# Optimization experiments

Measured on AMD Instinct MI355X. Metric: run time of the kernel, lower is better.

## Reference

```python
import jax, jax.numpy as jnp
import numpy as np

N_NODES = 8192
N_EDGES = 65536
NB = 10            # number_of_basis
MID = 32           # middle_layer_size
MAX_R = 10.0       # max_radius
NZ, NM = 48, 16    # z / mol embedding sizes -> 64x0e node input
IN_S = NZ + NM     # 64 scalars
H_S, H_V = 32, 8   # hidden irreps 32x0e + 8x1o (dim 56)
O_S = 16           # output irreps 16x0e
W0N = IN_S * H_S + IN_S * H_V                                  # 2560
W1N = H_S*H_S + H_V*H_S + H_S*H_V + H_V*H_V + H_V*H_V          # 1664
W2N = H_S*O_S + H_V*O_S                                        # 640
H_DIM = H_S + 3 * H_V                                          # 56


def _fcnet(e, W1, W2):
    # e3nn FullyConnectedNet([NB, MID, numel], silu): fan-in normalized linears
    h = jax.nn.silu(e @ W1 / np.sqrt(W1.shape[0]))
    return h @ W2 / np.sqrt(W2.shape[0])


def _ln(x, g, b):
    m = jnp.mean(x, -1, keepdims=True)
    v = jnp.var(x, -1, keepdims=True)
    return (x - m) * jax.lax.rsqrt(v + 1e-5) * g + b


def _sus(t):
    # smooth compact-support bump helper: exp(-1/t) for t>0 else 0
    return jnp.where(t > 0, jnp.exp(-1.0 / jnp.where(t > 0, t, 1.0)), 0.0)


def _forward(pos, Ez, Em,
             b0_W1, b0_W2, b0_g, b0_b,
             b1_W1, b1_W2, b1_g, b1_b,
             b2_W1, b2_W2, b2_g, b2_b,
             z, mol_id, edge_src, edge_dst):
    N = pos.shape[0]
    E = edge_src.shape[0]
    avg = E / N  # avg_num_neighbors (static)

    # node embedding: 64x0e
    x = jnp.concatenate([Ez[z], Em[mol_id]], axis=-1)          # [N, 64]

    vec = pos[edge_dst] - pos[edge_src]                        # [E, 3]
    length = jnp.linalg.norm(vec, axis=1)                      # [E]

    # soft_one_hot_linspace(basis='smooth_finite', cutoff=True) * sqrt(NB)
    vals = jnp.linspace(0.0, MAX_R, NB + 2)[1:-1]
    step = MAX_R / (NB + 1)
    u = (length[:, None] - vals) / step
    emb = (1.14136 * np.exp(2.0)) * _sus(u + 1.0) * _sus(1.0 - u)
    emb = emb * np.sqrt(NB)                                    # [E, NB]

    # spherical harmonics lmax=1, normalize=True, 'component' norm
    nrm = vec / jnp.maximum(length, 1e-9)[:, None]
    sh_v = np.sqrt(3.0) * nrm                                  # [E, 3]  (l=1; l=0 comp == 1)

    # ---- interaction block 0: 64x0e -> 32x0e + 8x1o ----
    w = _fcnet(emb, b0_W1, b0_W2)                              # [E, 2560]
    w00 = w[:, :IN_S * H_S].reshape(E, IN_S, H_S)
    w01 = w[:, IN_S * H_S:].reshape(E, IN_S, H_V)
    xe = x[edge_src]                                           # [E, 64]
    es = jnp.einsum('eu,euw->ew', xe, w00) / np.sqrt(IN_S)
    ev = jnp.einsum('eu,euw,ei->ewi', xe, w01, sh_v) / np.sqrt(IN_S)
    msg = jnp.concatenate([es, ev.reshape(E, 3 * H_V)], -1)    # [E, 56]
    x = _ln(jax.ops.segment_sum(msg, edge_dst, num_segments=N) / np.sqrt(avg), b0_g, b0_b)

    # ---- interaction block 1: 32x0e+8x1o -> 32x0e+8x1o ----
    w = _fcnet(emb, b1_W1, b1_W2)                              # [E, 1664]
    o = 0
    w_ss  = w[:, o:o + H_S*H_S].reshape(E, H_S, H_S); o += H_S*H_S
    w_vvs = w[:, o:o + H_V*H_S].reshape(E, H_V, H_S); o += H_V*H_S
    w_sv  = w[:, o:o + H_S*H_V].reshape(E, H_S, H_V); o += H_S*H_V
    w_vs  = w[:, o:o + H_V*H_V].reshape(E, H_V, H_V); o += H_V*H_V
    w_vvv = w[:, o:o + H_V*H_V].reshape(E, H_V, H_V)
    xs = x[:, :H_S][edge_src]                                  # [E, 32]
    xv = x[:, H_S:].reshape(N, H_V, 3)[edge_src]               # [E, 8, 3]
    dot = jnp.einsum('eui,ei->eu', xv, sh_v) / np.sqrt(3.0)    # 1o x 1o -> 0e CG
    crs = jnp.cross(xv, sh_v[:, None, :]) / np.sqrt(2.0)       # 1o x 1o -> 1o CG
    es = (jnp.einsum('eu,euw->ew', xs, w_ss) / np.sqrt(H_S)
          + jnp.einsum('eu,euw->ew', dot, w_vvs) / np.sqrt(H_V)) / np.sqrt(2.0)
    ev = (jnp.einsum('eu,euw,ei->ewi', xs, w_sv, sh_v) / np.sqrt(H_S)
          + jnp.einsum('eui,euw->ewi', xv, w_vs) / np.sqrt(H_V)
          + jnp.einsum('eui,euw->ewi', crs, w_vvv) / np.sqrt(H_V)) / np.sqrt(3.0)
    msg = jnp.concatenate([es, ev.reshape(E, 3 * H_V)], -1)
    x = _ln(jax.ops.segment_sum(msg, edge_dst, num_segments=N) / np.sqrt(avg), b1_g, b1_b)

    # ---- interaction block 2: 32x0e+8x1o -> 16x0e ----
    w = _fcnet(emb, b2_W1, b2_W2)                              # [E, 640]
    w_ss  = w[:, :H_S * O_S].reshape(E, H_S, O_S)
    w_vvs = w[:, H_S * O_S:].reshape(E, H_V, O_S)
    xs = x[:, :H_S][edge_src]
    xv = x[:, H_S:].reshape(N, H_V, 3)[edge_src]
    dot = jnp.einsum('eui,ei->eu', xv, sh_v) / np.sqrt(3.0)
    es = (jnp.einsum('eu,euw->ew', xs, w_ss) / np.sqrt(H_S)
          + jnp.einsum('eu,euw->ew', dot, w_vvs) / np.sqrt(H_V)) / np.sqrt(2.0)
    x = _ln(jax.ops.segment_sum(es, edge_dst, num_segments=N) / np.sqrt(avg), b2_g, b2_b)
    return x                                                   # [N, 16]


def setup_inputs():
    key = jax.random.key(0)
    ks = jax.random.split(key, 16)
    edge_src = jax.random.randint(ks[3], (N_EDGES,), 0, N_NODES)
    # exclude self-loops (radius_graph never returns them)
    edge_dst = (edge_src + 1 + jax.random.randint(ks[4], (N_EDGES,), 0, N_NODES - 1)) % N_NODES
    return {
        'pos': jax.random.uniform(ks[0], (N_NODES, 3), jnp.float32) * 8.0,
        'z': jax.random.randint(ks[1], (N_NODES,), 0, 100),
        'mol_id': jax.random.randint(ks[2], (N_NODES,), 0, 2),
        'edge_src': edge_src,
        'edge_dst': edge_dst,
        'Ez': jax.random.normal(ks[5], (100, NZ), jnp.float32),
        'Em': jax.random.normal(ks[6], (2, NM), jnp.float32),
        'b0_W1': jax.random.normal(ks[7], (NB, MID), jnp.float32),
        'b0_W2': jax.random.normal(ks[8], (MID, W0N), jnp.float32),
        'b0_g': jnp.ones((H_DIM,), jnp.float32),
        'b0_b': jnp.zeros((H_DIM,), jnp.float32),
        'b1_W1': jax.random.normal(ks[9], (NB, MID), jnp.float32),
        'b1_W2': jax.random.normal(ks[10], (MID, W1N), jnp.float32),
        'b1_g': jnp.ones((H_DIM,), jnp.float32),
        'b1_b': jnp.zeros((H_DIM,), jnp.float32),
        'b2_W1': jax.random.normal(ks[11], (NB, MID), jnp.float32),
        'b2_W2': jax.random.normal(ks[12], (MID, W2N), jnp.float32),
        'b2_g': jnp.ones((O_S,), jnp.float32),
        'b2_b': jnp.zeros((O_S,), jnp.float32),
    }


def reference(pos, z, mol_id, edge_src, edge_dst, Ez, Em,
              b0_W1, b0_W2, b0_g, b0_b,
              b1_W1, b1_W2, b1_g, b1_b,
              b2_W1, b2_W2, b2_g, b2_b):
    return _forward(pos, Ez, Em,
                    b0_W1, b0_W2, b0_g, b0_b,
                    b1_W1, b1_W2, b1_g, b1_b,
                    b2_W1, b2_W2, b2_g, b2_b,
                    z, mol_id, edge_src, edge_dst)
```

## Files before the change

### kernel.cpp

```cpp
#include <hip/hip_runtime.h>

#define NNODES 8192
#define NEDGES 65536

#define K_PACK   0.02209708691f
#define K_P1SV   0.01804219593f
#define K_VVS    0.04419417382f
#define K_VS     0.03608439182f
#define K_VVV    0.02551551815f
#define K_DOT    0.57735026919f
#define K_PRELN  0.35355339059f
#define C_EMB    8.4335730689f

typedef unsigned int uint32;
typedef unsigned short ushort16;
typedef __attribute__((ext_vector_type(8))) short short8;
typedef __attribute__((ext_vector_type(4))) float floatx4;

__device__ __forceinline__ float siluf(float x) { return x / (1.0f + __expf(-x)); }
__device__ __forceinline__ float susf(float t) { return t > 0.0f ? __expf(-1.0f / t) : 0.0f; }
__device__ __forceinline__ ushort16 f2bf(float f) {
  uint32 u = __float_as_uint(f);
  return (ushort16)((u + 0x7fffu + ((u >> 16) & 1u)) >> 16);
}
__device__ __forceinline__ float bflo(uint32 v) { return __uint_as_float(v << 16); }
__device__ __forceinline__ float bfhi(uint32 v) { return __uint_as_float(v & 0xffff0000u); }

__device__ __forceinline__ void mlp32(const float* __restrict__ W, const float emb[10],
                                      float* __restrict__ H) {
#pragma unroll
  for (int m = 0; m < 32; ++m) {
    float t = 0.f;
#pragma unroll
    for (int k = 0; k < 10; ++k) t += emb[k] * W[k * 32 + m];
    H[m] = siluf(t);
  }
}

__global__ __launch_bounds__(256) void k_prep(
    const float* __restrict__ pos, const int* __restrict__ z, const int* __restrict__ mol,
    const int* __restrict__ esrc, const int* __restrict__ edst,
    const float* __restrict__ Ez, const float* __restrict__ Em,
    const float* __restrict__ W10, const float* __restrict__ W11, const float* __restrict__ W12,
    const float* __restrict__ W20, const float* __restrict__ W21, const float* __restrict__ W22,
    int* __restrict__ combo, ushort16* __restrict__ X0cb, float* __restrict__ sh,
    float* __restrict__ h0, float* __restrict__ h1, float* __restrict__ h2,
    ushort16* __restrict__ h1b, ushort16* __restrict__ h2b,
    ushort16* __restrict__ Bp0, ushort16* __restrict__ Bp1, ushort16* __restrict__ Bp2,
    ushort16* __restrict__ Bpw1, ushort16* __restrict__ Bpw2, int* __restrict__ deg) {
  int idx = blockIdx.x * 256 + threadIdx.x;
  if (idx < NEDGES) {
    int e = idx;
    int s = esrc[e], d = edst[e];
    atomicAdd(&deg[d], 1);
    float vx = pos[d * 3 + 0] - pos[s * 3 + 0];
    float vy = pos[d * 3 + 1] - pos[s * 3 + 1];
    float vz = pos[d * 3 + 2] - pos[s * 3 + 2];
    float len = sqrtf(vx * vx + vy * vy + vz * vz);
    float inv = 1.7320508076f / fmaxf(len, 1e-9f);
    sh[e * 3 + 0] = vx * inv; sh[e * 3 + 1] = vy * inv; sh[e * 3 + 2] = vz * inv;
    float emb[10];
#pragma unroll
    for (int k = 0; k < 10; ++k) {
      float u = len * 1.1f - (float)(k + 1);
      emb[k] = C_EMB * susf(u + 1.0f) * susf(1.0f - u);
    }
    float H[32];
    mlp32(W10, emb, H);
#pragma unroll
    for (int m = 0; m < 32; ++m) h0[(size_t)e * 32 + m] = H[m];
    mlp32(W11, emb, H);
#pragma unroll
    for (int m = 0; m < 32; ++m) {
      h1[(size_t)e * 32 + m] = H[m];
      h1b[(size_t)e * 32 + m] = f2bf(H[m]);
    }
    mlp32(W12, emb, H);
#pragma unroll
    for (int m = 0; m < 32; ++m) {
      h2[(size_t)e * 32 + m] = H[m];
      h2b[(size_t)e * 32 + m] = f2bf(H[m]);
    }
    return;
  }
  idx -= NEDGES;
  if (idx < NNODES) { combo[idx] = z[idx] * 2 + mol[idx]; return; }
  idx -= NNODES;
  if (idx < 16384) {
    int c = idx >> 6, j = idx & 63;
    float v = 0.f;
    if (c < 200) {
      int zz = c >> 1, mm = c & 1;
      v = (j < 48) ? Ez[zz * 48 + j] : Em[mm * 16 + (j - 48)];
    }
    X0cb[idx] = f2bf(v);
    return;
  }
  idx -= 16384;
  if (idx < 81920) {
    int tile = idx >> 10; int r = idx & 1023;
    int kh = r >> 9; int rr = r & 511;
    int lane = rr >> 3, j = rr & 7;
    int k = kh * 32 + (lane >> 4) * 8 + j;
    int n = tile * 16 + (lane & 15);
    int c = n >> 5, m = n & 31;
    int col = (c < 32) ? (k * 32 + c) : (2048 + k * 8 + (c - 32));
    Bp0[idx] = f2bf(W20[m * 2560 + col] * K_PACK);
    return;
  }
  idx -= 81920;
  if (idx < 40960) {
    int tile = idx >> 9; int rr = idx & 511;
    int lane = rr >> 3, j = rr & 7;
    int k = (lane >> 4) * 8 + j;
    int n = tile * 16 + (lane & 15);
    int c = n >> 5, m = n & 31;
    float v = (c < 32) ? W21[m * 1664 + k * 32 + c] * K_PACK
                       : W21[m * 1664 + 1280 + k * 8 + (c - 32)] * K_P1SV;
    Bp1[idx] = f2bf(v);
    return;
  }
  idx -= 40960;
  if (idx < 16384) {
    int tile = idx >> 9; int rr = idx & 511;
    int lane = rr >> 3, j = rr & 7;
    int k = (lane >> 4) * 8 + j;
    int n = tile * 16 + (lane & 15);
    int c = n >> 5, m = n & 31;
    Bp2[idx] = f2bf(W22[m * 640 + k * 16 + c] * K_PACK);
    return;
  }
  idx -= 16384;
  if (idx < 12288) {
    int tile = idx >> 9; int rr = idx & 511;
    int lane = rr >> 3, j = rr & 7;
    int m = (lane >> 4) * 8 + j;
    int c = tile * 16 + (lane & 15);
    float v;
    if (c < 256) {
      int u = c >> 5, w = c & 31;
      v = W21[m * 1664 + 1024 + u * 32 + w] * K_VVS;
    } else {
      int r2 = c - 256; int t = r2 & 1; int l2 = r2 >> 1;
      int u = l2 >> 3, vv = l2 & 7;
      v = (t == 0) ? W21[m * 1664 + 1536 + u * 8 + vv] * K_VS
                   : W21[m * 1664 + 1600 + u * 8 + vv] * K_VVV;
    }
    Bpw1[idx] = f2bf(v);
    return;
  }
  idx -= 12288;
  {
    int tile = idx >> 9; int rr = idx & 511;
    int lane = rr >> 3, j = rr & 7;
    int m = (lane >> 4) * 8 + j;
    int c = tile * 16 + (lane & 15);
    int t = c & 1; int l2 = c >> 1;
    int u = l2 >> 3, wh = l2 & 7;
    Bpw2[idx] = f2bf(W22[m * 640 + 512 + u * 16 + wh * 2 + t] * K_VVS);
  }
}

__global__ __launch_bounds__(256) void k_scan(const int* __restrict__ deg,
                                              int* __restrict__ rowptr) {
  __shared__ int sums[256];
  int t = threadIdx.x;
  int base = t * 32;
  int local[32];
  int s = 0;
#pragma unroll
  for (int i = 0; i < 32; ++i) { local[i] = s; s += deg[base + i]; }
  sums[t] = s;
  __syncthreads();
  for (int off = 1; off < 256; off <<= 1) {
    int v = (t >= off) ? sums[t - off] : 0;
    __syncthreads();
    sums[t] += v;
    __syncthreads();
  }
  int prev = (t == 0) ? 0 : sums[t - 1];
#pragma unroll
  for (int i = 0; i < 32; ++i) rowptr[base + i] = prev + local[i];
  if (t == 255) rowptr[NNODES] = sums[255];
}

__global__ __launch_bounds__(256) void k_fill(const int* __restrict__ edst,
                                              const int* __restrict__ rowptr,
                                              int* __restrict__ fill, int* __restrict__ eidx) {
  int e = blockIdx.x * 256 + threadIdx.x;
  if (e >= NEDGES) return;
  int d = edst[e];
  int p = atomicAdd(&fill[d], 1);
  eidx[rowptr[d] + p] = e;
}

__global__ __launch_bounds__(256) void k_gemm_mfma(
    const ushort16* __restrict__ A, const ushort16* __restrict__ Bp, ushort16* __restrict__ C,
    int N, int K) {
  int wave = threadIdx.x >> 6, lane = threadIdx.x & 63;
  int m0 = blockIdx.x * 64 + wave * 16;
  int n0 = blockIdx.y * 64;
  int row = lane & 15, q = lane >> 4;
  int nkh = K >> 5;
  floatx4 acc[4];
  floatx4 zero = {0.f, 0.f, 0.f, 0.f};
#pragma unroll
  for (int t = 0; t < 4; ++t) acc[t] = zero;
  for (int kh = 0; kh < nkh; ++kh) {
    short8 a = *reinterpret_cast<const short8*>(A + (size_t)(m0 + row) * K + kh * 32 + q * 8);
#pragma unroll
    for (int t = 0; t < 4; ++t) {
      int T = (n0 >> 4) + t;
      short8 b = *reinterpret_cast<const short8*>(Bp + ((size_t)T * nkh + kh) * 512 + lane * 8);
      acc[t] = __builtin_amdgcn_mfma_f32_16x16x32_bf16(a, b, acc[t], 0, 0, 0);
    }
  }
  int colb = n0 + row;
#pragma unroll
  for (int t = 0; t < 4; ++t)
#pragma unroll
    for (int r = 0; r < 4; ++r)
      C[(size_t)(m0 + q * 4 + r) * N + colb + t * 16] = f2bf(acc[t][r]);
}

__global__ __launch_bounds__(256) void k_msg0(
    const int* __restrict__ rowmap, const int* __restrict__ esrc,
    const float* __restrict__ sh, const float* __restrict__ h,
    const ushort16* __restrict__ Pb, float* __restrict__ msg) {
  int e = __builtin_amdgcn_readfirstlane(blockIdx.x * 4 + (threadIdx.x >> 6));
  int lane = threadIdx.x & 63;
  int s = esrc[e];
  int row = rowmap[s];
  float sh0 = sh[e * 3 + 0], sh1 = sh[e * 3 + 1], sh2 = sh[e * 3 + 2];
  int c; float mult;
  if (lane < 32) { c = lane; mult = 1.0f; }
  else if (lane < 56) {
    int l = lane - 32; int v = l / 3; int i = l - v * 3;
    c = 32 + v;
    mult = (i == 0) ? sh0 : (i == 1 ? sh1 : sh2);
  } else { c = 0; mult = 0.0f; }
  const float* hp = h + (size_t)e * 32;
  const uint4* Pp = reinterpret_cast<const uint4*>(Pb + (size_t)row * 1280 + c * 32);
  float a = 0.f;
#pragma unroll
  for (int qq = 0; qq < 4; ++qq) {
    uint4 pv = Pp[qq];
    const float* hq = hp + qq * 8;
    a += bflo(pv.x) * hq[0] + bfhi(pv.x) * hq[1];
    a += bflo(pv.y) * hq[2] + bfhi(pv.y) * hq[3];
    a += bflo(pv.z) * hq[4] + bfhi(pv.z) * hq[5];
    a += bflo(pv.w) * hq[6] + bfhi(pv.w) * hq[7];
  }
  if (lane < 56) msg[(size_t)e * 56 + lane] = a * mult;
}

__global__ __launch_bounds__(256) void k_msg1(
    const int* __restrict__ esrc, const float* __restrict__ sh, const float* __restrict__ h,
    const ushort16* __restrict__ Pb, const float* __restrict__ xv,
    const ushort16* __restrict__ Wedge, float* __restrict__ msg) {
  __shared__ float vbuf[4][56];
  int w = threadIdx.x >> 6;
  int e = __builtin_amdgcn_readfirstlane(blockIdx.x * 4 + w);
  int lane = threadIdx.x & 63;
  int s = esrc[e];
  float sh0 = sh[e * 3 + 0], sh1 = sh[e * 3 + 1], sh2 = sh[e * 3 + 2];
  int u = lane >> 3;
  const float* xvp = xv + (size_t)s * 24 + u * 3;
  float x0 = xvp[0], x1 = xvp[1], x2 = xvp[2];
  float du = K_DOT * (x0 * sh0 + x1 * sh1 + x2 * sh2);
  float cr0 = x1 * sh2 - x2 * sh1;
  float cr1 = x2 * sh0 - x0 * sh2;
  float cr2 = x0 * sh1 - x1 * sh0;
  const ushort16* wp = Wedge + (size_t)e * 384;
  uint2 wv = *reinterpret_cast<const uint2*>(wp + lane * 4);
  uint32 wsv = *reinterpret_cast<const uint32*>(wp + 256 + lane * 2);
  float b0 = du * bflo(wv.x), b1 = du * bfhi(wv.x);
  float b2 = du * bflo(wv.y), b3 = du * bfhi(wv.y);
  float avs = bflo(wsv), avv = bfhi(wsv);
  float e0v = x0 * avs + cr0 * avv;
  float e1v = x1 * avs + cr1 * avv;
  float e2v = x2 * avs + cr2 * avv;
#pragma unroll
  for (int off = 8; off < 64; off <<= 1) {
    b0 += __shfl_xor(b0, off, 64); b1 += __shfl_xor(b1, off, 64);
    b2 += __shfl_xor(b2, off, 64); b3 += __shfl_xor(b3, off, 64);
    e0v += __shfl_xor(e0v, off, 64); e1v += __shfl_xor(e1v, off, 64);
    e2v += __shfl_xor(e2v, off, 64);
  }
  if (lane < 8) {
    vbuf[w][lane * 4 + 0] = b0; vbuf[w][lane * 4 + 1] = b1;
    vbuf[w][lane * 4 + 2] = b2; vbuf[w][lane * 4 + 3] = b3;
    vbuf[w][32 + lane * 3 + 0] = e0v;
    vbuf[w][32 + lane * 3 + 1] = e1v;
    vbuf[w][32 + lane * 3 + 2] = e2v;
  }
  int c; float mult;
  if (lane < 32) { c = lane; mult = 1.0f; }
  else if (lane < 56) {
    int l = lane - 32; int v = l / 3; int i = l - v * 3;
    c = 32 + v;
    mult = (i == 0) ? sh0 : (i == 1 ? sh1 : sh2);
  } else { c = 0; mult = 0.0f; }
  const float* hp = h + (size_t)e * 32;
  const uint4* Pp = reinterpret_cast<const uint4*>(Pb + (size_t)s * 1280 + c * 32);
  float a = 0.f;
#pragma unroll
  for (int qq = 0; qq < 4; ++qq) {
    uint4 pv = Pp[qq];
    const float* hq = hp + qq * 8;
    a += bflo(pv.x) * hq[0] + bfhi(pv.x) * hq[1];
    a += bflo(pv.y) * hq[2] + bfhi(pv.y) * hq[3];
    a += bflo(pv.z) * hq[4] + bfhi(pv.z) * hq[5];
    a += bflo(pv.w) * hq[6] + bfhi(pv.w) * hq[7];
  }
  __syncthreads();
  if (lane < 56) msg[(size_t)e * 56 + lane] = a * mult + vbuf[w][lane];
}

__global__ __launch_bounds__(256) void k_msg2(
    const int* __restrict__ esrc, const float* __restrict__ sh, const float* __restrict__ h,
    const ushort16* __restrict__ Pb, const float* __restrict__ xv,
    const ushort16* __restrict__ Wedge, float* __restrict__ msg) {
  __shared__ float vbuf[4][16];
  int w = threadIdx.x >> 6;
  int e = __builtin_amdgcn_readfirstlane(blockIdx.x * 4 + w);
  int lane = threadIdx.x & 63;
  int s = esrc[e];
  float sh0 = sh[e * 3 + 0], sh1 = sh[e * 3 + 1], sh2 = sh[e * 3 + 2];
  int u = lane >> 3;
  const float* xvp = xv + (size_t)s * 24 + u * 3;
  float du = K_DOT * (xvp[0] * sh0 + xvp[1] * sh1 + xvp[2] * sh2);
  uint32 w2 = *reinterpret_cast<const uint32*>(Wedge + (size_t)e * 128 + lane * 2);
  float c0 = du * bflo(w2), c1 = du * bfhi(w2);
#pragma unroll
  for (int off = 8; off < 64; off <<= 1) {
    c0 += __shfl_xor(c0, off, 64); c1 += __shfl_xor(c1, off, 64);
  }
  if (lane < 8) { vbuf[w][lane * 2 + 0] = c0; vbuf[w][lane * 2 + 1] = c1; }
  int q = lane >> 4, wc = lane & 15;
  const float* hq = h + (size_t)e * 32 + q * 8;
  uint4 pv = reinterpret_cast<const uint4*>(Pb + (size_t)s * 512 + wc * 32)[q];
  float a = bflo(pv.x) * hq[0] + bfhi(pv.x) * hq[1]
          + bflo(pv.y) * hq[2] + bfhi(pv.y) * hq[3]
          + bflo(pv.z) * hq[4] + bfhi(pv.z) * hq[5]
          + bflo(pv.w) * hq[6] + bfhi(pv.w) * hq[7];
  a += __shfl_xor(a, 16, 64);
  a += __shfl_xor(a, 32, 64);
  __syncthreads();
  if (lane < 16) msg[(size_t)e * 16 + lane] = a + vbuf[w][lane];
}

__global__ __launch_bounds__(256) void k_gather_ln(
    const int* __restrict__ rowptr, const int* __restrict__ eidx,
    const float* __restrict__ msg, int D,
    const float* __restrict__ g, const float* __restrict__ b,
    ushort16* __restrict__ xsb, float* __restrict__ xvf, float* __restrict__ outf) {
  int n = __builtin_amdgcn_readfirstlane(blockIdx.x * 4 + (threadIdx.x >> 6));
  int lane = threadIdx.x & 63;
  int r0 = rowptr[n], r1 = rowptr[n + 1];
  float v = 0.f;
  for (int j = r0; j < r1; ++j) {
    int e = eidx[j];
    if (lane < D) v += msg[(size_t)e * D + lane];
  }
  v *= K_PRELN;
  if (lane >= D) v = 0.f;
  float sm = v, sq = v * v;
#pragma unroll
  for (int off = 32; off > 0; off >>= 1) {
    sm += __shfl_xor(sm, off, 64);
    sq += __shfl_xor(sq, off, 64);
  }
  float invD = 1.0f / (float)D;
  float mean = sm * invD;
  float var = sq * invD - mean * mean;
  float rs = rsqrtf(var + 1e-5f);
  float r = (v - mean) * rs * g[lane < D ? lane : 0] + b[lane < D ? lane : 0];
  if (outf) {
    if (lane < D) outf[(size_t)n * D + lane] = r;
  } else {
    if (lane < 32) xsb[(size_t)n * 32 + lane] = f2bf(r);
    else if (lane < 56) xvf[(size_t)n * 24 + lane - 32] = r;
  }
}

extern "C" void kernel_launch(void* const* d_in, const int* in_sizes, int n_in,
                              void* d_out, int out_size, void* d_ws, size_t ws_size,
                              hipStream_t stream) {
  const float* pos = (const float*)d_in[0];
  const int* z = (const int*)d_in[1];
  const int* mol = (const int*)d_in[2];
  const int* esrc = (const int*)d_in[3];
  const int* edst = (const int*)d_in[4];
  const float* Ez = (const float*)d_in[5];
  const float* Em = (const float*)d_in[6];
  const float* b0W1 = (const float*)d_in[7];
  const float* b0W2 = (const float*)d_in[8];
  const float* b0g = (const float*)d_in[9];
  const float* b0b = (const float*)d_in[10];
  const float* b1W1 = (const float*)d_in[11];
  const float* b1W2 = (const float*)d_in[12];
  const float* b1g = (const float*)d_in[13];
  const float* b1b = (const float*)d_in[14];
  const float* b2W1 = (const float*)d_in[15];
  const float* b2W2 = (const float*)d_in[16];
  const float* b2g = (const float*)d_in[17];
  const float* b2b = (const float*)d_in[18];
  float* out = (float*)d_out;

  float* ws = (float*)d_ws;
  size_t o = 0;
  int* combo = (int*)(ws + o); o += NNODES;
  int* deg = (int*)(ws + o); o += NNODES;
  int* fill = (int*)(ws + o); o += NNODES;
  int* rowptr = (int*)(ws + o); o += NNODES + 8;
  int* eidx = (int*)(ws + o); o += NEDGES;
  ushort16* X0cb = (ushort16*)(ws + o); o += 8192;
  ushort16* xs1b = (ushort16*)(ws + o); o += 131072;
  float* xv1 = ws + o; o += (size_t)NNODES * 24;
  float* h0 = ws + o; o += (size_t)NEDGES * 32;
  float* h1 = ws + o; o += (size_t)NEDGES * 32;
  float* h2 = ws + o; o += (size_t)NEDGES * 32;
  float* shb = ws + o; o += (size_t)NEDGES * 3;
  ushort16* Bp0 = (ushort16*)(ws + o); o += 40960;
  ushort16* Bp1 = (ushort16*)(ws + o); o += 20480;
  ushort16* Bp2 = (ushort16*)(ws + o); o += 8192;
  ushort16* Bpw1 = (ushort16*)(ws + o); o += 6144;
  ushort16* Bpw2 = (ushort16*)(ws + o); o += 2048;
  ushort16* h1b = (ushort16*)(ws + o); o += (size_t)NEDGES * 16;
  ushort16* h2b = (ushort16*)(ws + o); o += (size_t)NEDGES * 16;
  ushort16* Wedge1 = (ushort16*)(ws + o); o += (size_t)NEDGES * 192;
  ushort16* P12 = (ushort16*)(ws + o); o += (size_t)NNODES * 640;
  float* msg56 = ws + o; o += (size_t)NEDGES * 56;

  ushort16* P0c = P12;
  ushort16* xs2b = xs1b;
  float* xv2 = xv1;
  ushort16* Wedge2 = Wedge1;
  float* msg16 = msg56;

  hipMemsetAsync(deg, 0, 2 * NNODES * sizeof(int), stream);

  k_prep<<<960, 256, 0, stream>>>(pos, z, mol, esrc, edst, Ez, Em,
                                  b0W1, b1W1, b2W1, b0W2, b1W2, b2W2,
                                  combo, X0cb, shb, h0, h1, h2, h1b, h2b,
                                  Bp0, Bp1, Bp2, Bpw1, Bpw2, deg);
  k_scan<<<1, 256, 0, stream>>>(deg, rowptr);
  k_fill<<<256, 256, 0, stream>>>(edst, rowptr, fill, eidx);

  k_gemm_mfma<<<dim3(4, 20), 256, 0, stream>>>(X0cb, Bp0, P0c, 1280, 64);
  k_gemm_mfma<<<dim3(1024, 6), 256, 0, stream>>>(h1b, Bpw1, Wedge1, 384, 32);
  k_msg0<<<16384, 256, 0, stream>>>(combo, esrc, shb, h0, P0c, msg56);
  k_gather_ln<<<2048, 256, 0, stream>>>(rowptr, eidx, msg56, 56, b0g, b0b, xs1b, xv1, nullptr);

  k_gemm_mfma<<<dim3(128, 20), 256, 0, stream>>>(xs1b, Bp1, P12, 1280, 32);
  k_msg1<<<16384, 256, 0, stream>>>(esrc, shb, h1, P12, xv1, Wedge1, msg56);
  k_gather_ln<<<2048, 256, 0, stream>>>(rowptr, eidx, msg56, 56, b1g, b1b, xs2b, xv2, nullptr);

  k_gemm_mfma<<<dim3(1024, 2), 256, 0, stream>>>(h2b, Bpw2, Wedge2, 128, 32);
  k_gemm_mfma<<<dim3(128, 8), 256, 0, stream>>>(xs2b, Bp2, P12, 512, 32);
  k_msg2<<<16384, 256, 0, stream>>>(esrc, shb, h2, P12, xv2, Wedge2, msg16);
  k_gather_ln<<<2048, 256, 0, stream>>>(rowptr, eidx, msg16, 16, b2g, b2b, nullptr, nullptr, out);
}
```

Before: 254.2 us.

## Compute messages per source node via source-sorted CSR to reuse node operands

Adds a second CSR keyed by source node (degree counts, scan and fill for both directions). The three message kernels now assign one wave per source node, load that node's projected weights and vector features into registers once, and loop over its outgoing edges. The per-edge weight layouts (Bpw1/Bpw2) are permuted so each lane reads contiguous 8-element chunks instead of doing cross-lane shuffle reductions. This aims to cut redundant gathers of per-node data and the shuffle/LDS reduction work, at the risk of load imbalance from variable out-degree and serial edge loops with scattered msg writes.

```diff
diff --git a/kernel.cpp b/kernel.cpp
--- a/kernel.cpp
+++ b/kernel.cpp
@@ -53,6 +53,7 @@
     int e = idx;
     int s = esrc[e], d = edst[e];
     atomicAdd(&deg[d], 1);
+    atomicAdd(&deg[NNODES + s], 1);
     float vx = pos[d * 3 + 0] - pos[s * 3 + 0];
     float vy = pos[d * 3 + 1] - pos[s * 3 + 1];
     float vz = pos[d * 3 + 2] - pos[s * 3 + 2];
@@ -135,16 +136,17 @@
     int tile = idx >> 9; int rr = idx & 511;
     int lane = rr >> 3, j = rr & 7;
     int m = (lane >> 4) * 8 + j;
-    int c = tile * 16 + (lane & 15);
+    int n = tile * 16 + (lane & 15);
     float v;
-    if (c < 256) {
-      int u = c >> 5, w = c & 31;
-      v = W21[m * 1664 + 1024 + u * 32 + w] * K_VVS;
+    if (n < 256) {
+      int c = n >> 3, u = n & 7;
+      v = W21[m * 1664 + 1024 + u * 32 + c] * K_VVS;
+    } else if (n < 320) {
+      int vo = (n - 256) >> 3, u = n & 7;
+      v = W21[m * 1664 + 1536 + u * 8 + vo] * K_VS;
     } else {
-      int r2 = c - 256; int t = r2 & 1; int l2 = r2 >> 1;
-      int u = l2 >> 3, vv = l2 & 7;
-      v = (t == 0) ? W21[m * 1664 + 1536 + u * 8 + vv] * K_VS
-                   : W21[m * 1664 + 1600 + u * 8 + vv] * K_VVV;
+      int vo = (n - 320) >> 3, u = n & 7;
+      v = W21[m * 1664 + 1600 + u * 8 + vo] * K_VVV;
     }
     Bpw1[idx] = f2bf(v);
     return;
@@ -154,22 +156,23 @@
     int tile = idx >> 9; int rr = idx & 511;
     int lane = rr >> 3, j = rr & 7;
     int m = (lane >> 4) * 8 + j;
-    int c = tile * 16 + (lane & 15);
-    int t = c & 1; int l2 = c >> 1;
-    int u = l2 >> 3, wh = l2 & 7;
-    Bpw2[idx] = f2bf(W22[m * 640 + 512 + u * 16 + wh * 2 + t] * K_VVS);
+    int n = tile * 16 + (lane & 15);
+    int c = n >> 3, u = n & 7;
+    Bpw2[idx] = f2bf(W22[m * 640 + 512 + u * 16 + c] * K_VVS);
   }
 }
 
 __global__ __launch_bounds__(256) void k_scan(const int* __restrict__ deg,
                                               int* __restrict__ rowptr) {
+  const int* in = deg + blockIdx.x * NNODES;
+  int* out = rowptr + blockIdx.x * (NNODES + 1);
   __shared__ int sums[256];
   int t = threadIdx.x;
   int base = t * 32;
   int local[32];
   int s = 0;
 #pragma unroll
-  for (int i = 0; i < 32; ++i) { local[i] = s; s += deg[base + i]; }
+  for (int i = 0; i < 32; ++i) { local[i] = s; s += in[base + i]; }
   sums[t] = s;
   __syncthreads();
   for (int off = 1; off < 256; off <<= 1) {
@@ -180,18 +183,26 @@
   }
   int prev = (t == 0) ? 0 : sums[t - 1];
 #pragma unroll
-  for (int i = 0; i < 32; ++i) rowptr[base + i] = prev + local[i];
-  if (t == 255) rowptr[NNODES] = sums[255];
-}
-
-__global__ __launch_bounds__(256) void k_fill(const int* __restrict__ edst,
-                                              const int* __restrict__ rowptr,
-                                              int* __restrict__ fill, int* __restrict__ eidx) {
-  int e = blockIdx.x * 256 + threadIdx.x;
-  if (e >= NEDGES) return;
-  int d = edst[e];
-  int p = atomicAdd(&fill[d], 1);
-  eidx[rowptr[d] + p] = e;
+  for (int i = 0; i < 32; ++i) out[base + i] = prev + local[i];
+  if (t == 255) out[NNODES] = sums[255];
+}
+
+__global__ __launch_bounds__(256) void k_fill(
+    const int* __restrict__ esrc, const int* __restrict__ edst,
+    const int* __restrict__ rowptr, int* __restrict__ fill, int* __restrict__ eidx) {
+  int t = blockIdx.x * 256 + threadIdx.x;
+  if (t < NEDGES) {
+    int d = edst[t];
+    int p = atomicAdd(&fill[d], 1);
+    eidx[rowptr[d] + p] = t;
+  } else {
+    int e = t - NEDGES;
+    if (e < NEDGES) {
+      int s = esrc[e];
+      int p = atomicAdd(&fill[NNODES + s], 1);
+      eidx[NEDGES + rowptr[NNODES + 1 + s] + p] = e;
+    }
+  }
 }
 
 __global__ __launch_bounds__(256) void k_gemm_mfma(
@@ -223,131 +234,139 @@
       C[(size_t)(m0 + q * 4 + r) * N + colb + t * 16] = f2bf(acc[t][r]);
 }
 
-__global__ __launch_bounds__(256) void k_msg0(
-    const int* __restrict__ rowmap, const int* __restrict__ esrc,
+__global__ __launch_bounds__(256) void k_msg0n(
+    const int* __restrict__ rowptr_s, const int* __restrict__ eidx_s,
+    const int* __restrict__ combo, const float* __restrict__ sh,
+    const float* __restrict__ h, const ushort16* __restrict__ Pb, float* __restrict__ msg) {
+  int n = __builtin_amdgcn_readfirstlane(blockIdx.x * 4 + (threadIdx.x >> 6));
+  int lane = threadIdx.x & 63;
+  int l = lane - 32;
+  int vi = (l >= 0) ? ((l / 3 > 7) ? 7 : l / 3) : 0;
+  int ii = (l >= 0) ? (l - (l / 3) * 3) : 0;
+  int cp = (lane < 32) ? lane : 32 + vi;
+  int row = combo[n];
+  const uint4* Pp = reinterpret_cast<const uint4*>(Pb + (size_t)row * 1280 + cp * 32);
+  uint4 P0 = Pp[0], P1 = Pp[1], P2 = Pp[2], P3 = Pp[3];
+  int r0 = rowptr_s[n], r1 = rowptr_s[n + 1];
+  for (int j = r0; j < r1; ++j) {
+    int e = __builtin_amdgcn_readfirstlane(eidx_s[j]);
+    float sh0 = sh[e * 3 + 0], sh1 = sh[e * 3 + 1], sh2 = sh[e * 3 + 2];
+    const float* hp = h + (size_t)e * 32;
+    float a = 0.f;
+    a += bflo(P0.x) * hp[0] + bfhi(P0.x) * hp[1] + bflo(P0.y) * hp[2] + bfhi(P0.y) * hp[3];
+    a += bflo(P0.z) * hp[4] + bfhi(P0.z) * hp[5] + bflo(P0.w) * hp[6] + bfhi(P0.w) * hp[7];
+    a += bflo(P1.x) * hp[8] + bfhi(P1.x) * hp[9] + bflo(P1.y) * hp[10] + bfhi(P1.y) * hp[11];
+    a += bflo(P1.z) * hp[12] + bfhi(P1.z) * hp[13] + bflo(P1.w) * hp[14] + bfhi(P1.w) * hp[15];
+    a += bflo(P2.x) * hp[16] + bfhi(P2.x) * hp[17] + bflo(P2.y) * hp[18] + bfhi(P2.y) * hp[19];
+    a += bflo(P2.z) * hp[20] + bfhi(P2.z) * hp[21] + bflo(P2.w) * hp[22] + bfhi(P2.w) * hp[23];
+    a += bflo(P3.x) * hp[24] + bfhi(P3.x) * hp[25] + bflo(P3.y) * hp[26] + bfhi(P3.y) * hp[27];
+    a += bflo(P3.z) * hp[28] + bfhi(P3.z) * hp[29] + bflo(P3.w) * hp[30] + bfhi(P3.w) * hp[31];
+    float mult = (lane < 32) ? 1.0f : ((ii == 0) ? sh0 : (ii == 1) ? sh1 : sh2);
+    if (lane < 56) msg[(size_t)e * 56 + lane] = a * mult;
+  }
+}
+
+__global__ __launch_bounds__(256) void k_msg1n(
+    const int* __restrict__ rowptr_s, const int* __restrict__ eidx_s,
     const float* __restrict__ sh, const float* __restrict__ h,
-    const ushort16* __restrict__ Pb, float* __restrict__ msg) {
-  int e = __builtin_amdgcn_readfirstlane(blockIdx.x * 4 + (threadIdx.x >> 6));
-  int lane = threadIdx.x & 63;
-  int s = esrc[e];
-  int row = rowmap[s];
-  float sh0 = sh[e * 3 + 0], sh1 = sh[e * 3 + 1], sh2 = sh[e * 3 + 2];
-  int c; float mult;
-  if (lane < 32) { c = lane; mult = 1.0f; }
-  else if (lane < 56) {
-    int l = lane - 32; int v = l / 3; int i = l - v * 3;
-    c = 32 + v;
-    mult = (i == 0) ? sh0 : (i == 1 ? sh1 : sh2);
-  } else { c = 0; mult = 0.0f; }
-  const float* hp = h + (size_t)e * 32;
-  const uint4* Pp = reinterpret_cast<const uint4*>(Pb + (size_t)row * 1280 + c * 32);
-  float a = 0.f;
-#pragma unroll
-  for (int qq = 0; qq < 4; ++qq) {
-    uint4 pv = Pp[qq];
-    const float* hq = hp + qq * 8;
-    a += bflo(pv.x) * hq[0] + bfhi(pv.x) * hq[1];
-    a += bflo(pv.y) * hq[2] + bfhi(pv.y) * hq[3];
-    a += bflo(pv.z) * hq[4] + bfhi(pv.z) * hq[5];
-    a += bflo(pv.w) * hq[6] + bfhi(pv.w) * hq[7];
-  }
-  if (lane < 56) msg[(size_t)e * 56 + lane] = a * mult;
-}
-
-__global__ __launch_bounds__(256) void k_msg1(
-    const int* __restrict__ esrc, const float* __restrict__ sh, const float* __restrict__ h,
     const ushort16* __restrict__ Pb, const float* __restrict__ xv,
     const ushort16* __restrict__ Wedge, float* __restrict__ msg) {
-  __shared__ float vbuf[4][56];
-  int w = threadIdx.x >> 6;
-  int e = __builtin_amdgcn_readfirstlane(blockIdx.x * 4 + w);
+  int n = __builtin_amdgcn_readfirstlane(blockIdx.x * 4 + (threadIdx.x >> 6));
   int lane = threadIdx.x & 63;
-  int s = esrc[e];
-  float sh0 = sh[e * 3 + 0], sh1 = sh[e * 3 + 1], sh2 = sh[e * 3 + 2];
-  int u = lane >> 3;
-  const float* xvp = xv + (size_t)s * 24 + u * 3;
-  float x0 = xvp[0], x1 = xvp[1], x2 = xvp[2];
-  float du = K_DOT * (x0 * sh0 + x1 * sh1 + x2 * sh2);
-  float cr0 = x1 * sh2 - x2 * sh1;
-  float cr1 = x2 * sh0 - x0 * sh2;
-  float cr2 = x0 * sh1 - x1 * sh0;
-  const ushort16* wp = Wedge + (size_t)e * 384;
-  uint2 wv = *reinterpret_cast<const uint2*>(wp + lane * 4);
-  uint32 wsv = *reinterpret_cast<const uint32*>(wp + 256 + lane * 2);
-  float b0 = du * bflo(wv.x), b1 = du * bfhi(wv.x);
-  float b2 = du * bflo(wv.y), b3 = du * bfhi(wv.y);
-  float avs = bflo(wsv), avv = bfhi(wsv);
-  float e0v = x0 * avs + cr0 * avv;
-  float e1v = x1 * avs + cr1 * avv;
-  float e2v = x2 * avs + cr2 * avv;
-#pragma unroll
-  for (int off = 8; off < 64; off <<= 1) {
-    b0 += __shfl_xor(b0, off, 64); b1 += __shfl_xor(b1, off, 64);
-    b2 += __shfl_xor(b2, off, 64); b3 += __shfl_xor(b3, off, 64);
-    e0v += __shfl_xor(e0v, off, 64); e1v += __shfl_xor(e1v, off, 64);
-    e2v += __shfl_xor(e2v, off, 64);
-  }
-  if (lane < 8) {
-    vbuf[w][lane * 4 + 0] = b0; vbuf[w][lane * 4 + 1] = b1;
-    vbuf[w][lane * 4 + 2] = b2; vbuf[w][lane * 4 + 3] = b3;
-    vbuf[w][32 + lane * 3 + 0] = e0v;
-    vbuf[w][32 + lane * 3 + 1] = e1v;
-    vbuf[w][32 + lane * 3 + 2] = e2v;
-  }
-  int c; float mult;
-  if (lane < 32) { c = lane; mult = 1.0f; }
-  else if (lane < 56) {
-    int l = lane - 32; int v = l / 3; int i = l - v * 3;
-    c = 32 + v;
-    mult = (i == 0) ? sh0 : (i == 1 ? sh1 : sh2);
-  } else { c = 0; mult = 0.0f; }
-  const float* hp = h + (size_t)e * 32;
-  const uint4* Pp = reinterpret_cast<const uint4*>(Pb + (size_t)s * 1280 + c * 32);
-  float a = 0.f;
-#pragma unroll
-  for (int qq = 0; qq < 4; ++qq) {
-    uint4 pv = Pp[qq];
-    const float* hq = hp + qq * 8;
-    a += bflo(pv.x) * hq[0] + bfhi(pv.x) * hq[1];
-    a += bflo(pv.y) * hq[2] + bfhi(pv.y) * hq[3];
-    a += bflo(pv.z) * hq[4] + bfhi(pv.z) * hq[5];
-    a += bflo(pv.w) * hq[6] + bfhi(pv.w) * hq[7];
-  }
-  __syncthreads();
-  if (lane < 56) msg[(size_t)e * 56 + lane] = a * mult + vbuf[w][lane];
-}
-
-__global__ __launch_bounds__(256) void k_msg2(
-    const int* __restrict__ esrc, const float* __restrict__ sh, const float* __restrict__ h,
+  int l = lane - 32;
+  int vi = (l >= 0) ? ((l / 3 > 7) ? 7 : l / 3) : 0;
+  int ii = (l >= 0) ? (l - (l / 3) * 3) : 0;
+  int cp = (lane < 32) ? lane : 32 + vi;
+  const uint4* Pp = reinterpret_cast<const uint4*>(Pb + (size_t)n * 1280 + cp * 32);
+  uint4 P0 = Pp[0], P1 = Pp[1], P2 = Pp[2], P3 = Pp[3];
+  const float* xvp = xv + (size_t)n * 24;
+  float xr[24];
+#pragma unroll
+  for (int t = 0; t < 24; ++t) xr[t] = xvp[t];
+  int r0 = rowptr_s[n], r1 = rowptr_s[n + 1];
+  for (int j = r0; j < r1; ++j) {
+    int e = __builtin_amdgcn_readfirstlane(eidx_s[j]);
+    float sh0 = sh[e * 3 + 0], sh1 = sh[e * 3 + 1], sh2 = sh[e * 3 + 2];
+    const float* hp = h + (size_t)e * 32;
+    float a = 0.f;
+    a += bflo(P0.x) * hp[0] + bfhi(P0.x) * hp[1] + bflo(P0.y) * hp[2] + bfhi(P0.y) * hp[3];
+    a += bflo(P0.z) * hp[4] + bfhi(P0.z) * hp[5] + bflo(P0.w) * hp[6] + bfhi(P0.w) * hp[7];
+    a += bflo(P1.x) * hp[8] + bfhi(P1.x) * hp[9] + bflo(P1.y) * hp[10] + bfhi(P1.y) * hp[11];
+    a += bflo(P1.z) * hp[12] + bfhi(P1.z) * hp[13] + bflo(P1.w) * hp[14] + bfhi(P1.w) * hp[15];
+    a += bflo(P2.x) * hp[16] + bfhi(P2.x) * hp[17] + bflo(P2.y) * hp[18] + bfhi(P2.y) * hp[19];
+    a += bflo(P2.z) * hp[20] + bfhi(P2.z) * hp[21] + bflo(P2.w) * hp[22] + bfhi(P2.w) * hp[23];
+    a += bflo(P3.x) * hp[24] + bfhi(P3.x) * hp[25] + bflo(P3.y) * hp[26] + bfhi(P3.y) * hp[27];
+    a += bflo(P3.z) * hp[28] + bfhi(P3.z) * hp[29] + bflo(P3.w) * hp[30] + bfhi(P3.w) * hp[31];
+    const ushort16* wp = Wedge + (size_t)e * 384;
+    float vterm, mult;
+    if (lane < 32) {
+      mult = 1.0f;
+      float du[8];
+#pragma unroll
+      for (int u = 0; u < 8; ++u)
+        du[u] = K_DOT * (xr[u * 3] * sh0 + xr[u * 3 + 1] * sh1 + xr[u * 3 + 2] * sh2);
+      uint4 wv = *reinterpret_cast<const uint4*>(wp + lane * 8);
+      vterm = du[0] * bflo(wv.x) + du[1] * bfhi(wv.x) + du[2] * bflo(wv.y) + du[3] * bfhi(wv.y)
+            + du[4] * bflo(wv.z) + du[5] * bfhi(wv.z) + du[6] * bflo(wv.w) + du[7] * bfhi(wv.w);
+    } else {
+      float shi = (ii == 0) ? sh0 : (ii == 1) ? sh1 : sh2;
+      float s1 = (ii == 0) ? sh1 : (ii == 1) ? sh2 : sh0;
+      float s2 = (ii == 0) ? sh2 : (ii == 1) ? sh0 : sh1;
+      mult = shi;
+      uint4 wvs = *reinterpret_cast<const uint4*>(wp + 256 + vi * 8);
+      uint4 wvv = *reinterpret_cast<const uint4*>(wp + 320 + vi * 8);
+      float vsw[8] = {bflo(wvs.x), bfhi(wvs.x), bflo(wvs.y), bfhi(wvs.y),
+                      bflo(wvs.z), bfhi(wvs.z), bflo(wvs.w), bfhi(wvs.w)};
+      float vvw[8] = {bflo(wvv.x), bfhi(wvv.x), bflo(wvv.y), bfhi(wvv.y),
+                      bflo(wvv.z), bfhi(wvv.z), bflo(wvv.w), bfhi(wvv.w)};
+      vterm = 0.f;
+#pragma unroll
+      for (int u = 0; u < 8; ++u) {
+        float xu0 = xr[u * 3], xu1 = xr[u * 3 + 1], xu2 = xr[u * 3 + 2];
+        float xui = (ii == 0) ? xu0 : (ii == 1) ? xu1 : xu2;
+        float xi1 = (ii == 0) ? xu1 : (ii == 1) ? xu2 : xu0;
+        float xi2 = (ii == 0) ? xu2 : (ii == 1) ? xu0 : xu1;
+        float crs = xi1 * s2 - xi2 * s1;
+        vterm += xui * vsw[u] + crs * vvw[u];
+      }
+    }
+    if (lane < 56) msg[(size_t)e * 56 + lane] = a * mult + vterm;
+  }
+}
+
+__global__ __launch_bounds__(256) void k_msg2n(
+    const int* __restrict__ rowptr_s, const int* __restrict__ eidx_s,
+    const float* __restrict__ sh, const float* __restrict__ h,
     const ushort16* __restrict__ Pb, const float* __restrict__ xv,
     const ushort16* __restrict__ Wedge, float* __restrict__ msg) {
-  __shared__ float vbuf[4][16];
-  int w = threadIdx.x >> 6;
-  int e = __builtin_amdgcn_readfirstlane(blockIdx.x * 4 + w);
+  int n = __builtin_amdgcn_readfirstlane(blockIdx.x * 4 + (threadIdx.x >> 6));
   int lane = threadIdx.x & 63;
-  int s = esrc[e];
-  float sh0 = sh[e * 3 + 0], sh1 = sh[e * 3 + 1], sh2 = sh[e * 3 + 2];
-  int u = lane >> 3;
-  const float* xvp = xv + (size_t)s * 24 + u * 3;
-  float du = K_DOT * (xvp[0] * sh0 + xvp[1] * sh1 + xvp[2] * sh2);
-  uint32 w2 = *reinterpret_cast<const uint32*>(Wedge + (size_t)e * 128 + lane * 2);
-  float c0 = du * bflo(w2), c1 = du * bfhi(w2);
-#pragma unroll
-  for (int off = 8; off < 64; off <<= 1) {
-    c0 += __shfl_xor(c0, off, 64); c1 += __shfl_xor(c1, off, 64);
-  }
-  if (lane < 8) { vbuf[w][lane * 2 + 0] = c0; vbuf[w][lane * 2 + 1] = c1; }
-  int q = lane >> 4, wc = lane & 15;
-  const float* hq = h + (size_t)e * 32 + q * 8;
-  uint4 pv = reinterpret_cast<const uint4*>(Pb + (size_t)s * 512 + wc * 32)[q];
-  float a = bflo(pv.x) * hq[0] + bfhi(pv.x) * hq[1]
-          + bflo(pv.y) * hq[2] + bfhi(pv.y) * hq[3]
-          + bflo(pv.z) * hq[4] + bfhi(pv.z) * hq[5]
-          + bflo(pv.w) * hq[6] + bfhi(pv.w) * hq[7];
-  a += __shfl_xor(a, 16, 64);
-  a += __shfl_xor(a, 32, 64);
-  __syncthreads();
-  if (lane < 16) msg[(size_t)e * 16 + lane] = a + vbuf[w][lane];
+  int c = lane & 15, q = lane >> 4;
+  uint4 Pq = *reinterpret_cast<const uint4*>(Pb + (size_t)n * 512 + c * 32 + q * 8);
+  const float* xvp = xv + (size_t)n * 24;
+  float xr[24];
+#pragma unroll
+  for (int t = 0; t < 24; ++t) xr[t] = xvp[t];
+  int r0 = rowptr_s[n], r1 = rowptr_s[n + 1];
+  for (int j = r0; j < r1; ++j) {
+    int e = __builtin_amdgcn_readfirstlane(eidx_s[j]);
+    float sh0 = sh[e * 3 + 0], sh1 = sh[e * 3 + 1], sh2 = sh[e * 3 + 2];
+    const float* hq = h + (size_t)e * 32 + q * 8;
+    float a = bflo(Pq.x) * hq[0] + bfhi(Pq.x) * hq[1]
+            + bflo(Pq.y) * hq[2] + bfhi(Pq.y) * hq[3]
+            + bflo(Pq.z) * hq[4] + bfhi(Pq.z) * hq[5]
+            + bflo(Pq.w) * hq[6] + bfhi(Pq.w) * hq[7];
+    a += __shfl_xor(a, 16, 64);
+    a += __shfl_xor(a, 32, 64);
+    float du[8];
+#pragma unroll
+    for (int u = 0; u < 8; ++u)
+      du[u] = K_DOT * (xr[u * 3] * sh0 + xr[u * 3 + 1] * sh1 + xr[u * 3 + 2] * sh2);
+    uint4 wv = *reinterpret_cast<const uint4*>(Wedge + (size_t)e * 128 + c * 8);
+    float vterm = du[0] * bflo(wv.x) + du[1] * bfhi(wv.x) + du[2] * bflo(wv.y) + du[3] * bfhi(wv.y)
+                + du[4] * bflo(wv.z) + du[5] * bfhi(wv.z) + du[6] * bflo(wv.w) + du[7] * bfhi(wv.w);
+    if (lane < 16) msg[(size_t)e * 16 + c] = a + vterm;
+  }
 }
 
 __global__ __launch_bounds__(256) void k_gather_ln(
@@ -411,10 +430,10 @@
   float* ws = (float*)d_ws;
   size_t o = 0;
   int* combo = (int*)(ws + o); o += NNODES;
-  int* deg = (int*)(ws + o); o += NNODES;
-  int* fill = (int*)(ws + o); o += NNODES;
-  int* rowptr = (int*)(ws + o); o += NNODES + 8;
-  int* eidx = (int*)(ws + o); o += NEDGES;
+  int* deg = (int*)(ws + o); o += 2 * NNODES;
+  int* fill = (int*)(ws + o); o += 2 * NNODES;
+  int* rowptr = (int*)(ws + o); o += 2 * (NNODES + 1) + 6;
+  int* eidx = (int*)(ws + o); o += 2 * NEDGES;
   ushort16* X0cb = (ushort16*)(ws + o); o += 8192;
   ushort16* xs1b = (ushort16*)(ws + o); o += 131072;
   float* xv1 = ws + o; o += (size_t)NNODES * 24;
@@ -433,32 +452,34 @@
   ushort16* P12 = (ushort16*)(ws + o); o += (size_t)NNODES * 640;
   float* msg56 = ws + o; o += (size_t)NEDGES * 56;
 
+  int* rowptr_s = rowptr + NNODES + 1;
+  int* eidx_s = eidx + NEDGES;
   ushort16* P0c = P12;
   ushort16* xs2b = xs1b;
   float* xv2 = xv1;
   ushort16* Wedge2 = Wedge1;
   float* msg16 = msg56;
 
-  hipMemsetAsync(deg, 0, 2 * NNODES * sizeof(int), stream);
+  hipMemsetAsync(deg, 0, 4 * NNODES * sizeof(int), stream);
 
   k_prep<<<960, 256, 0, stream>>>(pos, z, mol, esrc, edst, Ez, Em,
                                   b0W1, b1W1, b2W1, b0W2, b1W2, b2W2,
                                   combo, X0cb, shb, h0, h1, h2, h1b, h2b,
                                   Bp0, Bp1, Bp2, Bpw1, Bpw2, deg);
-  k_scan<<<1, 256, 0, stream>>>(deg, rowptr);
-  k_fill<<<256, 256, 0, stream>>>(edst, rowptr, fill, eidx);
+  k_scan<<<2, 256, 0, stream>>>(deg, rowptr);
+  k_fill<<<512, 256, 0, stream>>>(esrc, edst, rowptr, fill, eidx);
 
   k_gemm_mfma<<<dim3(4, 20), 256, 0, stream>>>(X0cb, Bp0, P0c, 1280, 64);
   k_gemm_mfma<<<dim3(1024, 6), 256, 0, stream>>>(h1b, Bpw1, Wedge1, 384, 32);
-  k_msg0<<<16384, 256, 0, stream>>>(combo, esrc, shb, h0, P0c, msg56);
+  k_msg0n<<<2048, 256, 0, stream>>>(rowptr_s, eidx_s, combo, shb, h0, P0c, msg56);
   k_gather_ln<<<2048, 256, 0, stream>>>(rowptr, eidx, msg56, 56, b0g, b0b, xs1b, xv1, nullptr);
 
   k_gemm_mfma<<<dim3(128, 20), 256, 0, stream>>>(xs1b, Bp1, P12, 1280, 32);
-  k_msg1<<<16384, 256, 0, stream>>>(esrc, shb, h1, P12, xv1, Wedge1, msg56);
+  k_msg1n<<<2048, 256, 0, stream>>>(rowptr_s, eidx_s, shb, h1, P12, xv1, Wedge1, msg56);
   k_gather_ln<<<2048, 256, 0, stream>>>(rowptr, eidx, msg56, 56, b1g, b1b, xs2b, xv2, nullptr);
 
   k_gemm_mfma<<<dim3(1024, 2), 256, 0, stream>>>(h2b, Bpw2, Wedge2, 128, 32);
   k_gemm_mfma<<<dim3(128, 8), 256, 0, stream>>>(xs2b, Bp2, P12, 512, 32);
-  k_msg2<<<16384, 256, 0, stream>>>(esrc, shb, h2, P12, xv2, Wedge2, msg16);
+  k_msg2n<<<2048, 256, 0, stream>>>(rowptr_s, eidx_s, shb, h2, P12, xv2, Wedge2, msg16);
   k_gather_ln<<<2048, 256, 0, stream>>>(rowptr, eidx, msg16, 16, b2g, b2b, nullptr, nullptr, out);
 }
```

Result: slower. 263.6 us (+3.7%).
